# Kernel optimization log

Hardware: AMD Instinct MI355X
Metric: run time of the kernel (lower is better)

Reference implementation:

```python
import jax, jax.numpy as jnp
import numpy as np

SIGMA_MAX = 0.3
GAMMA = 1.0
COV_SHRINK = 0.1
COV_DELTA = 1e-3
BN_EPS = 1e-5
PATCH = 3


def setup_inputs() -> dict:
    key = jax.random.key(0)
    ks = jax.random.split(key, 5)
    B, K, C, H, W = 2, 8, 64, 128, 128
    X = jax.random.normal(ks[0], (B, K, C, H, W), dtype=jnp.float32)
    w1 = jax.random.normal(ks[1], (C // 2, C), dtype=jnp.float32) * 0.1
    w2 = jax.random.normal(ks[2], (1, C // 2), dtype=jnp.float32) * 0.1
    return {
        "X": X,
        "w1": w1,
        "bn_scale": jnp.ones((C // 2,), jnp.float32),
        "bn_bias": jnp.zeros((C // 2,), jnp.float32),
        "bn_mean": jnp.zeros((C // 2,), jnp.float32),
        "bn_var": jnp.ones((C // 2,), jnp.float32),
        "w2": w2,
        "a0_raw": jax.random.normal(ks[3], (K,), dtype=jnp.float32) * 0.1,
        "sigma_raw": jax.random.normal(ks[4], (K,), dtype=jnp.float32) * 0.1,
    }


def _forward(X, w1, bn_scale, bn_bias, bn_mean, bn_var, w2, a0_raw, sigma_raw):
    B, K, C, H, W = X.shape
    # --- SensorMapGenerator: 1x1 conv -> BN (inference) -> ReLU -> 1x1 conv ---
    Xf = X.reshape(B * K, C, H, W)
    h = jnp.einsum('oc,bchw->bohw', w1, Xf)                       # [BK, C/2, H, W]
    inv_std = bn_scale / jnp.sqrt(bn_var + BN_EPS)
    h = h * inv_std[None, :, None, None] + (bn_bias - bn_mean * inv_std)[None, :, None, None]
    h = jax.nn.relu(h)
    S = jnp.einsum('oc,bchw->bohw', w2, h).reshape(B, K, H, W)    # scalar sensor maps

    # --- CovarianceEstimator: reflect pad, 3x3 patches, center, R = PP^T/N ---
    pad = PATCH // 2
    Sp = jnp.pad(S, ((0, 0), (0, 0), (pad, pad), (pad, pad)), mode='reflect')
    patches = jnp.stack(
        [Sp[:, :, i:i + H, j:j + W] for i in range(PATCH) for j in range(PATCH)],
        axis=-1)                                                  # [B, K, H, W, N]
    N = PATCH * PATCH
    patches = patches.transpose(0, 2, 3, 1, 4)                    # [B, H, W, K, N]
    pc = patches - patches.mean(axis=-1, keepdims=True)
    R = jnp.matmul(pc, pc.swapaxes(-1, -2)) / N                   # [B, H, W, K, K]

    # --- Guidance vector and uncertainty (stage mode) ---
    a0 = jax.nn.softmax(a0_raw)                                   # [K], sums to 1
    sigma = SIGMA_MAX * jax.nn.sigmoid(sigma_raw)                 # [K]

    # --- Robust diagonal-loaded Capon solve per pixel ---
    # R_reg = (1-shrink)*R + shrink*(tr R / K)*I + delta*I + gamma*diag(sigma^2)
    I = jnp.eye(K, dtype=R.dtype)
    tr = jnp.trace(R, axis1=-2, axis2=-1)                         # [B, H, W]
    load = COV_DELTA * I + GAMMA * jnp.diag(sigma * sigma)
    R_load = (1.0 - COV_SHRINK) * R + (COV_SHRINK * tr / K)[..., None, None] * I + load
    rhs = jnp.broadcast_to(a0[:, None], R_load.shape[:-2] + (K, 1))
    w_un = jnp.linalg.solve(R_load, rhs)[..., 0]                  # [B, H, W, K]
    denom = jnp.einsum('bhwk,k->bhw', w_un, a0)
    w = w_un / denom[..., None]                                   # a0^T w = 1

    # --- Weighted fusion over streams ---
    Y = jnp.einsum('bhwk,bkchw->bchw', w, X)                      # [B, C, H, W]
    return Y


def reference(X, w1, bn_scale, bn_bias, bn_mean, bn_var, w2, a0_raw, sigma_raw):
    return _forward(X, w1, bn_scale, bn_bias, bn_mean, bn_var, w2, a0_raw, sigma_raw)
```

## Files before the change

kernel.cpp:

```cpp
#include <hip/hip_runtime.h>
#include <math.h>

#define B_    2
#define K_    8
#define C_    64
#define CH_   32
#define H_    128
#define W_    128
#define HW_   16384
#define BN_EPS 1e-5f
#define SIGMA_MAX 0.3f
#define COV_SHRINK 0.1f
#define COV_DELTA 1e-3f

#define TILE_ 64

__global__ void prep_kernel(const float* __restrict__ w1,
                            const float* __restrict__ bn_scale,
                            const float* __restrict__ bn_bias,
                            const float* __restrict__ bn_mean,
                            const float* __restrict__ bn_var,
                            const float* __restrict__ w2,
                            const float* __restrict__ a0_raw,
                            const float* __restrict__ sigma_raw,
                            float* __restrict__ par) {
    int t = threadIdx.x;
    for (int i = t; i < CH_ * C_; i += blockDim.x) {
        int c = i >> 5;
        int o = i & 31;
        float inv = bn_scale[o] / sqrtf(bn_var[o] + BN_EPS);
        par[c * CH_ + o] = w1[o * C_ + c] * inv;
    }
    if (t < CH_) {
        float inv = bn_scale[t] / sqrtf(bn_var[t] + BN_EPS);
        par[2048 + t] = bn_bias[t] - bn_mean[t] * inv;
        par[2080 + t] = w2[t];
    }
    if (t < K_) {
        float m = -1e30f;
        for (int i = 0; i < K_; ++i) m = fmaxf(m, a0_raw[i]);
        float s = 0.f;
        for (int i = 0; i < K_; ++i) s += expf(a0_raw[i] - m);
        par[2112 + t] = expf(a0_raw[t] - m) / s;
        float sg = SIGMA_MAX / (1.f + expf(-sigma_raw[t]));
        par[2120 + t] = sg * sg;
    }
}

__global__ void __launch_bounds__(256)
stage1_kernel(const float* __restrict__ X,
              const float* __restrict__ wf,
              const float* __restrict__ beff,
              const float* __restrict__ w2,
              float* __restrict__ S) {
    int idx = blockIdx.x * blockDim.x + threadIdx.x;
    int hw2 = idx & (HW_ / 2 - 1);
    int bk  = idx >> 13;
    const float* xp = X + (size_t)bk * (C_ * HW_) + (size_t)hw2 * 2;

    float a0c[CH_], a1c[CH_];
#pragma unroll
    for (int o = 0; o < CH_; ++o) {
        float b = beff[o];
        a0c[o] = b;
        a1c[o] = b;
    }

#pragma unroll 4
    for (int c = 0; c < C_; ++c) {
        float2 xv = *(const float2*)(xp + (size_t)c * HW_);
        const float* wrow = wf + c * CH_;
#pragma unroll
        for (int o = 0; o < CH_; ++o) {
            float wv = wrow[o];
            a0c[o] = fmaf(wv, xv.x, a0c[o]);
            a1c[o] = fmaf(wv, xv.y, a1c[o]);
        }
    }
    float s0 = 0.f, s1 = 0.f;
#pragma unroll
    for (int o = 0; o < CH_; ++o) {
        float wv = w2[o];
        s0 = fmaf(wv, fmaxf(a0c[o], 0.f), s0);
        s1 = fmaf(wv, fmaxf(a1c[o], 0.f), s1);
    }
    *(float2*)(S + (size_t)idx * 2) = make_float2(s0, s1);
}

__global__ void __launch_bounds__(256)
capon_fuse_kernel(const float* __restrict__ X,
                  const float* __restrict__ S,
                  const float* __restrict__ a0,
                  const float* __restrict__ sig2,
                  float* __restrict__ out) {
    __shared__ float wL[TILE_][K_ + 1];

    int tid   = threadIdx.x;
    int gbase = blockIdx.x * TILE_;
    int b      = gbase >> 14;
    int hwbase = gbase & (HW_ - 1);

    if (tid < TILE_) {
        int hw = hwbase + tid;
        int h  = hw >> 7;
        int w  = hw & (W_ - 1);

        int hm = (h == 0)      ? 1      : h - 1;
        int hp = (h == H_ - 1) ? H_ - 2 : h + 1;
        int wm = (w == 0)      ? 1      : w - 1;
        int wp = (w == W_ - 1) ? W_ - 2 : w + 1;
        int rows[3] = {hm * W_, h * W_, hp * W_};
        int cols[3] = {wm, w, wp};

        float pc[K_][9];
#pragma unroll
        for (int k = 0; k < K_; ++k) {
            const float* sp = S + (((size_t)b * K_ + k) << 14);
            float p[9];
            float m = 0.f;
#pragma unroll
            for (int i = 0; i < 3; ++i)
#pragma unroll
                for (int j = 0; j < 3; ++j) {
                    float v = sp[rows[i] + cols[j]];
                    p[i * 3 + j] = v;
                    m += v;
                }
            m *= (1.f / 9.f);
#pragma unroll
            for (int n = 0; n < 9; ++n) pc[k][n] = p[n] - m;
        }

        float A[K_][K_];
        float tr = 0.f;
#pragma unroll
        for (int i = 0; i < K_; ++i) {
            float s = 0.f;
#pragma unroll
            for (int n = 0; n < 9; ++n) s = fmaf(pc[i][n], pc[i][n], s);
            s *= (1.f / 9.f);
            tr += s;
            A[i][i] = s;
        }
#pragma unroll
        for (int i = 0; i < K_; ++i)
#pragma unroll
            for (int j = 0; j < i; ++j) {
                float s = 0.f;
#pragma unroll
                for (int n = 0; n < 9; ++n) s = fmaf(pc[i][n], pc[j][n], s);
                A[i][j] = (1.f - COV_SHRINK) * s * (1.f / 9.f);
            }
        float dl = COV_SHRINK * tr * (1.f / (float)K_) + COV_DELTA;
#pragma unroll
        for (int i = 0; i < K_; ++i)
            A[i][i] = (1.f - COV_SHRINK) * A[i][i] + dl + sig2[i];

#pragma unroll
        for (int j = 0; j < K_; ++j) {
            float d = A[j][j];
#pragma unroll
            for (int t = 0; t < j; ++t) d = fmaf(-A[j][t], A[j][t], d);
            d = sqrtf(d);
            A[j][j] = d;
            float inv = 1.f / d;
#pragma unroll
            for (int i = j + 1; i < K_; ++i) {
                float s = A[i][j];
#pragma unroll
                for (int t = 0; t < j; ++t) s = fmaf(-A[i][t], A[j][t], s);
                A[i][j] = s * inv;
            }
        }
        float z[K_];
#pragma unroll
        for (int i = 0; i < K_; ++i) {
            float s = a0[i];
#pragma unroll
            for (int t = 0; t < i; ++t) s = fmaf(-A[i][t], z[t], s);
            z[i] = s / A[i][i];
        }
        float x[K_];
#pragma unroll
        for (int i = K_ - 1; i >= 0; --i) {
            float s = z[i];
#pragma unroll
            for (int t = i + 1; t < K_; ++t) s = fmaf(-A[t][i], x[t], s);
            x[i] = s / A[i][i];
        }
        float denom = 0.f;
#pragma unroll
        for (int k = 0; k < K_; ++k) denom = fmaf(x[k], a0[k], denom);
        float invd = 1.f / denom;
#pragma unroll
        for (int k = 0; k < K_; ++k) wL[tid][k] = x[k] * invd;
    }
    __syncthreads();

    int px = tid & (TILE_ - 1);
    int c4 = tid >> 6;
    float wr[K_];
#pragma unroll
    for (int k = 0; k < K_; ++k) wr[k] = wL[px][k];

    const float* xb = X + ((size_t)b * K_ * C_) * HW_ + hwbase + px;
    float* ob = out + ((size_t)b * C_) * HW_ + hwbase + px;
    const size_t kstride = (size_t)C_ * HW_;

#pragma unroll 4
    for (int cc = 0; cc < C_ / 4; ++cc) {
        int c = (cc << 2) | c4;
        const float* xp = xb + (size_t)c * HW_;
        float acc = wr[0] * xp[0];
        acc = fmaf(wr[1], xp[kstride * 1], acc);
        acc = fmaf(wr[2], xp[kstride * 2], acc);
        acc = fmaf(wr[3], xp[kstride * 3], acc);
        acc = fmaf(wr[4], xp[kstride * 4], acc);
        acc = fmaf(wr[5], xp[kstride * 5], acc);
        acc = fmaf(wr[6], xp[kstride * 6], acc);
        acc = fmaf(wr[7], xp[kstride * 7], acc);
        ob[(size_t)c * HW_] = acc;
    }
}

extern "C" void kernel_launch(void* const* d_in, const int* in_sizes, int n_in,
                              void* d_out, int out_size, void* d_ws, size_t ws_size,
                              hipStream_t stream) {
    const float* X         = (const float*)d_in[0];
    const float* w1        = (const float*)d_in[1];
    const float* bn_scale  = (const float*)d_in[2];
    const float* bn_bias   = (const float*)d_in[3];
    const float* bn_mean   = (const float*)d_in[4];
    const float* bn_var    = (const float*)d_in[5];
    const float* w2        = (const float*)d_in[6];
    const float* a0_raw    = (const float*)d_in[7];
    const float* sigma_raw = (const float*)d_in[8];
    float* out = (float*)d_out;
    float* ws  = (float*)d_ws;

    float* par = ws;
    float* S   = ws + 4096;

    prep_kernel<<<1, 256, 0, stream>>>(w1, bn_scale, bn_bias, bn_mean, bn_var,
                                       w2, a0_raw, sigma_raw, par);

    int n1 = B_ * K_ * HW_ / 2;
    stage1_kernel<<<n1 / 256, 256, 0, stream>>>(X, par, par + 2048, par + 2080, S);

    int n2 = B_ * HW_ / TILE_;
    capon_fuse_kernel<<<n2, 256, 0, stream>>>(X, S, par + 2112, par + 2120, out);
}
```

Baseline: 159.0 us.

## Split stage1 channel reduction across two wavefronts per pixel with LDS combine

Stage1 now gives each thread one pixel and half of the input channels, so two wavefronts cooperate on each pixel. Their partial 32-wide accumulators are combined through shared memory before ReLU and the second projection. This cuts per-thread registers (32 accumulators instead of 64) and raises the thread count fourfold to improve occupancy and latency hiding, with launch bounds requesting 8 blocks per CU. In exchange it adds an LDS round trip and a block barrier, and half the threads sit idle during the final reduction.

```diff
diff --git a/kernel.cpp b/kernel.cpp
--- a/kernel.cpp
+++ b/kernel.cpp
@@ -47,44 +47,55 @@
     }
 }
 
-__global__ void __launch_bounds__(256)
+__global__ void __launch_bounds__(256, 8)
 stage1_kernel(const float* __restrict__ X,
               const float* __restrict__ wf,
               const float* __restrict__ beff,
               const float* __restrict__ w2,
               float* __restrict__ S) {
-    int idx = blockIdx.x * blockDim.x + threadIdx.x;
-    int hw2 = idx & (HW_ / 2 - 1);
-    int bk  = idx >> 13;
-    const float* xp = X + (size_t)bk * (C_ * HW_) + (size_t)hw2 * 2;
-
-    float a0c[CH_], a1c[CH_];
-#pragma unroll
-    for (int o = 0; o < CH_; ++o) {
-        float b = beff[o];
-        a0c[o] = b;
-        a1c[o] = b;
+    __shared__ float xch[2][64][CH_ + 1];
+
+    int tid  = threadIdx.x;
+    int lane = tid & 63;
+    int pair = tid >> 7;
+    int half = (tid >> 6) & 1;
+    int gpx  = blockIdx.x * 128 + pair * 64 + lane;
+    int bk   = gpx >> 14;
+    int hw   = gpx & (HW_ - 1);
+    const float* xp = X + (size_t)bk * (C_ * HW_) + hw;
+    int cbase = __builtin_amdgcn_readfirstlane(half << 5);
+
+    float acc[CH_];
+    if (half == 0) {
+#pragma unroll
+        for (int o = 0; o < CH_; ++o) acc[o] = beff[o];
+    } else {
+#pragma unroll
+        for (int o = 0; o < CH_; ++o) acc[o] = 0.f;
     }
 
 #pragma unroll 4
-    for (int c = 0; c < C_; ++c) {
-        float2 xv = *(const float2*)(xp + (size_t)c * HW_);
-        const float* wrow = wf + c * CH_;
+    for (int c = 0; c < CH_; ++c) {
+        float xv = xp[(size_t)(cbase + c) * HW_];
+        const float* wrow = wf + (cbase + c) * CH_;
+#pragma unroll
+        for (int o = 0; o < CH_; ++o) acc[o] = fmaf(wrow[o], xv, acc[o]);
+    }
+
+    if (half == 1) {
+#pragma unroll
+        for (int o = 0; o < CH_; ++o) xch[pair][lane][o] = acc[o];
+    }
+    __syncthreads();
+    if (half == 0) {
+        float s = 0.f;
 #pragma unroll
         for (int o = 0; o < CH_; ++o) {
-            float wv = wrow[o];
-            a0c[o] = fmaf(wv, xv.x, a0c[o]);
-            a1c[o] = fmaf(wv, xv.y, a1c[o]);
-        }
-    }
-    float s0 = 0.f, s1 = 0.f;
-#pragma unroll
-    for (int o = 0; o < CH_; ++o) {
-        float wv = w2[o];
-        s0 = fmaf(wv, fmaxf(a0c[o], 0.f), s0);
-        s1 = fmaf(wv, fmaxf(a1c[o], 0.f), s1);
-    }
-    *(float2*)(S + (size_t)idx * 2) = make_float2(s0, s1);
+            float v = acc[o] + xch[pair][lane][o];
+            s = fmaf(w2[o], fmaxf(v, 0.f), s);
+        }
+        S[gpx] = s;
+    }
 }
 
 __global__ void __launch_bounds__(256)
@@ -244,7 +255,7 @@
     prep_kernel<<<1, 256, 0, stream>>>(w1, bn_scale, bn_bias, bn_mean, bn_var,
                                        w2, a0_raw, sigma_raw, par);
 
-    int n1 = B_ * K_ * HW_ / 2;
+    int n1 = B_ * K_ * HW_ * 2;
     stage1_kernel<<<n1 / 256, 256, 0, stream>>>(X, par, par + 2048, par + 2080, S);
 
     int n2 = B_ * HW_ / TILE_;
```

Result: faster. 132.6 us (-16.6%).
